# Kernel optimization log

Hardware: AMD Instinct MI355X
Metric: run time of the kernel (lower is better)

The kernel has to match this reference:

```python
import jax, jax.numpy as jnp
import numpy as np

GS = 128          # r_group_size
Q_MAX = 7.0       # 2**(q_bits-1)-1, q_bits=4
R_MAX = 7.0       # 2**(r_bits-1)-1, r_bits=4
R_MIN = -8.0      # -R_MAX-1
EPS = 1e-8


def _fake_quant_group(w, n_bits=4, group_size=128, eps=1e-8):
    # symmetric group-wise fake quant of the weight (done once at __init__)
    qmax = 2 ** (n_bits - 1) - 1
    qmin = -qmax - 1
    O, I = w.shape
    wg = w.reshape(O, I // group_size, group_size)
    scale = jnp.maximum(jnp.max(jnp.abs(wg), axis=-1, keepdims=True) / qmax, eps)
    wq = jnp.clip(jnp.round(wg / scale), qmin, qmax) * scale
    return wq.reshape(O, I)


def _select_pow2_base(t):
    # smallest value in {2,4,8,16,32,64} that is >= t (64 if none)
    base = jnp.full_like(t, 64.0)
    for v in (32.0, 16.0, 8.0, 4.0, 2.0):
        base = jnp.where(t <= v, jnp.full_like(t, v), base)
    return base


def setup_inputs() -> dict:
    key = jax.random.key(0)
    kx, kw, kb = jax.random.split(key, 3)
    B, S, IN, OUT = 4, 2048, 4096, 11008
    x = jax.random.normal(kx, (B, S, IN), dtype=jnp.float32)
    w_raw = jax.random.normal(kw, (OUT, IN), dtype=jnp.float32)
    weight = _fake_quant_group(w_raw, n_bits=4, group_size=128)
    bias = jax.random.normal(kb, (OUT,), dtype=jnp.float32)
    return {"x": x, "weight": weight, "bias": bias}


def reference(x, weight, bias):
    # dynamic quotient-remainder activation fake-quant (init path)
    H = x.shape[-1]
    xg = x.astype(jnp.float32).reshape(x.shape[:-1] + (H // GS, GS))  # [..., G, gs]
    max_abs = jnp.maximum(jnp.max(jnp.abs(xg), axis=-1, keepdims=True), EPS)
    base = _select_pow2_base(max_abs / Q_MAX)                 # [..., G, 1]
    q = jnp.clip(jnp.round(xg / base), -Q_MAX, Q_MAX)          # quotient
    r = xg - base * q                                          # remainder
    max_abs_r = jnp.maximum(jnp.max(jnp.abs(r), axis=-1, keepdims=True), EPS)
    scale_r = max_abs_r / R_MAX
    r_dq = jnp.clip(jnp.round(r / scale_r), R_MIN, R_MAX) * scale_r
    x_recon = (base * q + r_dq).reshape(x.shape)
    # F.linear: y = x @ W^T + b
    return jnp.einsum("bsi,oi->bso", x_recon, weight) + bias
```

## Files before the change

kernel.cpp:

```cpp
#include <hip/hip_runtime.h>
#include <stdint.h>
#include <stddef.h>

typedef __bf16 bf16x8 __attribute__((ext_vector_type(8)));
typedef float  f32x4  __attribute__((ext_vector_type(4)));
typedef float  f32x2  __attribute__((ext_vector_type(2)));

__device__ __forceinline__ unsigned short f2bf(float f) {
  unsigned int u = __builtin_bit_cast(unsigned int, f);
  u += 0x7fffu + ((u >> 16) & 1u);
  return (unsigned short)(u >> 16);
}

__device__ __forceinline__ void gld_lds16(const void* g, void* l) {
  __builtin_amdgcn_global_load_lds(
      (__attribute__((address_space(1))) void*)(g),
      (__attribute__((address_space(3))) void*)(l), 16, 0, 0);
}

#define BAR()     asm volatile("s_barrier" ::: "memory")
#define WAITVM(n) asm volatile("s_waitcnt vmcnt(" #n ")" ::: "memory")
#define SCHED0()  __builtin_amdgcn_sched_barrier(0)

__global__ __launch_bounds__(256) void quant_x_kernel(
    const float* __restrict__ x, unsigned short* __restrict__ xb, long long ngroups)
{
  const int lane = threadIdx.x & 63;
  const int wv   = threadIdx.x >> 6;
  long long g = (long long)blockIdx.x * 4 + wv;
  if (g >= ngroups) return;

  const float* xg = x + g * 128;
  f32x2 v = __builtin_nontemporal_load(
      reinterpret_cast<const f32x2*>(xg + lane * 2));

  float m = fmaxf(fabsf(v[0]), fabsf(v[1]));
  #pragma unroll
  for (int off = 32; off; off >>= 1) m = fmaxf(m, __shfl_xor(m, off));
  m = fmaxf(m, 1e-8f);

  float t = m / 7.0f;
  float base = t <= 2.f ? 2.f : t <= 4.f ? 4.f : t <= 8.f ? 8.f
             : t <= 16.f ? 16.f : t <= 32.f ? 32.f : 64.f;
  float inv_base = 1.0f / base;

  float q0 = fminf(fmaxf(rintf(v[0] * inv_base), -7.f), 7.f);
  float q1 = fminf(fmaxf(rintf(v[1] * inv_base), -7.f), 7.f);
  float r0 = v[0] - base * q0;
  float r1 = v[1] - base * q1;

  float mr = fmaxf(fabsf(r0), fabsf(r1));
  #pragma unroll
  for (int off = 32; off; off >>= 1) mr = fmaxf(mr, __shfl_xor(mr, off));
  mr = fmaxf(mr, 1e-8f);
  float scale_r = mr / 7.0f;

  float rd0 = fminf(fmaxf(rintf(r0 / scale_r), -8.f), 7.f) * scale_r;
  float rd1 = fminf(fmaxf(rintf(r1 / scale_r), -8.f), 7.f) * scale_r;

  float y0 = base * q0 + rd0;
  float y1 = base * q1 + rd1;

  unsigned int packed = (unsigned int)f2bf(y0) | ((unsigned int)f2bf(y1) << 16);
  *reinterpret_cast<unsigned int*>(xb + g * 128 + lane * 2) = packed;
}

__global__ __launch_bounds__(256) void cvt_w_kernel(
    const float* __restrict__ w, unsigned short* __restrict__ wb, long long n)
{
  long long i = ((long long)blockIdx.x * blockDim.x + threadIdx.x) * 8;
  if (i + 7 >= n) {
    if (i >= n) return;
    for (long long j = i; j < n; ++j) wb[j] = f2bf(w[j]);
    return;
  }
  f32x4 v0 = __builtin_nontemporal_load(reinterpret_cast<const f32x4*>(w + i));
  f32x4 v1 = __builtin_nontemporal_load(reinterpret_cast<const f32x4*>(w + i + 4));
  uint4 o;
  o.x = (unsigned)f2bf(v0[0]) | ((unsigned)f2bf(v0[1]) << 16);
  o.y = (unsigned)f2bf(v0[2]) | ((unsigned)f2bf(v0[3]) << 16);
  o.z = (unsigned)f2bf(v1[0]) | ((unsigned)f2bf(v1[1]) << 16);
  o.w = (unsigned)f2bf(v1[2]) | ((unsigned)f2bf(v1[3]) << 16);
  *reinterpret_cast<uint4*>(wb + i) = o;
}

#define BM 256
#define BN 256
#define BK 64

#define MFMA16(a, b, c) __builtin_amdgcn_mfma_f32_16x16x32_bf16(a, b, c, 0, 0, 0)

__global__ __launch_bounds__(512, 2) void gemm256_bias(
    const unsigned short* __restrict__ A,
    const unsigned short* __restrict__ B,
    const float* __restrict__ bias,
    float* __restrict__ C,
    int M, int N, int K)
{
  __shared__ unsigned short lds[2][2][2][128 * 64];

  const int tid  = threadIdx.x;
  const int lane = tid & 63;
  const int wid  = tid >> 6;
  const int wm   = wid >> 2;
  const int wn   = wid & 3;
  const int laneq = lane & 15;
  const int laneh = lane >> 4;
  const int lq7   = laneq & 7;

  const int ntm = M / BM;
  const int ntn = N / BN;
  int tm, tn;
  if ((ntm & 15) == 0) {
    int rem = blockIdx.x;
    int str = 0, stc = 0, w = 16;
    for (;;) {
      int w2 = (ntn - stc * 16 < 16) ? (ntn - stc * 16) : 16;
      int sz = 16 * w2;
      if (rem < sz) { w = w2; break; }
      rem -= sz;
      ++stc;
      if (stc * 16 >= ntn) { stc = 0; ++str; }
    }
    tm = str * 16 + rem / w;
    tn = stc * 16 + rem % w;
  } else {
    tm = (int)blockIdx.x / ntn;
    tn = (int)blockIdx.x % ntn;
  }
  const size_t m0 = (size_t)tm * BM;
  const size_t n0 = (size_t)tn * BN;

  const int NT = K / BK;

  const int ss0 = (laneh ^ lq7);
  const int ss1 = ((4 + laneh) ^ lq7);

  const char* ldsb = (const char*)&lds[0][0][0][0];
  const int aOff = wm * 16384 + laneq * 128;
  const int bOff = 32768 + (wn >> 1) * 16384 + ((wn & 1) * 64 + laneq) * 128;

  const int c0 = tid, c1 = 512 + tid;
  const int r0 = c0 >> 3, sl0 = (c0 & 7) ^ (r0 & 7);
  const int r1 = c1 >> 3, sl1 = (c1 & 7) ^ (r1 & 7);
  const unsigned short* gA0 = A + (m0 + r0) * (size_t)K + sl0 * 8;
  const unsigned short* gA1 = A + (m0 + r1) * (size_t)K + sl1 * 8;
  const unsigned short* gB0 = B + (n0 + r0) * (size_t)K + sl0 * 8;
  const unsigned short* gB1 = B + (n0 + r1) * (size_t)K + sl1 * 8;
  const size_t hstep = (size_t)128 * K;

  char* dst0 = (char*)ldsb + wid * 1024;
  char* dst1 = dst0 + 65536;

  f32x4 acc[8][4];
  #pragma unroll
  for (int i = 0; i < 8; i++)
    #pragma unroll
    for (int j = 0; j < 4; j++)
      acc[i][j] = (f32x4){0.f, 0.f, 0.f, 0.f};

  #define STAGETILE(kt, dstD)                                                \
    do {                                                                     \
      gld_lds16(gA0 + (size_t)(kt) * 64,          (dstD));                   \
      gld_lds16(gA1 + (size_t)(kt) * 64,          (dstD) + 8192);            \
      gld_lds16(gA0 + hstep + (size_t)(kt) * 64,  (dstD) + 16384);           \
      gld_lds16(gA1 + hstep + (size_t)(kt) * 64,  (dstD) + 16384 + 8192);    \
      gld_lds16(gB0 + (size_t)(kt) * 64,          (dstD) + 32768);           \
      gld_lds16(gB1 + (size_t)(kt) * 64,          (dstD) + 32768 + 8192);    \
      gld_lds16(gB0 + hstep + (size_t)(kt) * 64,  (dstD) + 49152);           \
      gld_lds16(gB1 + hstep + (size_t)(kt) * 64,  (dstD) + 49152 + 8192);    \
    } while (0)

  STAGETILE(0, dst0);
  WAITVM(0);
  BAR();

  bf16x8 al[4][2], ah[4][2], bl[2][2], bh[2][2];

  for (int t = 0; t < NT; ++t) {
    const int d = t & 1;
    const char* aS0 = ldsb + (d << 16) + aOff + ss0 * 16;
    const char* aS1 = ldsb + (d << 16) + aOff + ss1 * 16;
    const char* bS0 = ldsb + (d << 16) + bOff + ss0 * 16;
    const char* bS1 = ldsb + (d << 16) + bOff + ss1 * 16;

    if (t + 1 < NT) { char* dn = d ? dst0 : dst1; STAGETILE(t + 1, dn); }

    #pragma unroll
    for (int mi = 0; mi < 4; ++mi) {
      al[mi][0] = *(const bf16x8*)(aS0 + mi * 2048);
      al[mi][1] = *(const bf16x8*)(aS1 + mi * 2048);
    }
    #pragma unroll
    for (int nj = 0; nj < 2; ++nj) {
      bl[nj][0] = *(const bf16x8*)(bS0 + nj * 2048);
      bl[nj][1] = *(const bf16x8*)(bS1 + nj * 2048);
    }
    #pragma unroll
    for (int nj = 0; nj < 2; ++nj) {
      bh[nj][0] = *(const bf16x8*)(bS0 + 4096 + nj * 2048);
      bh[nj][1] = *(const bf16x8*)(bS1 + 4096 + nj * 2048);
    }
    #pragma unroll
    for (int mi = 0; mi < 4; ++mi) {
      ah[mi][0] = *(const bf16x8*)(aS0 + 8192 + mi * 2048);
      ah[mi][1] = *(const bf16x8*)(aS1 + 8192 + mi * 2048);
    }
    SCHED0();

    __builtin_amdgcn_s_setprio(1);
    #pragma unroll
    for (int mi = 0; mi < 4; ++mi)
      #pragma unroll
      for (int nj = 0; nj < 2; ++nj) {
        acc[mi][nj] = MFMA16(al[mi][0], bl[nj][0], acc[mi][nj]);
        acc[mi][nj] = MFMA16(al[mi][1], bl[nj][1], acc[mi][nj]);
      }
    SCHED0();
    #pragma unroll
    for (int mi = 0; mi < 4; ++mi)
      #pragma unroll
      for (int nj = 0; nj < 2; ++nj) {
        acc[mi][2 + nj] = MFMA16(al[mi][0], bh[nj][0], acc[mi][2 + nj]);
        acc[mi][2 + nj] = MFMA16(al[mi][1], bh[nj][1], acc[mi][2 + nj]);
      }
    SCHED0();
    #pragma unroll
    for (int mi = 0; mi < 4; ++mi)
      #pragma unroll
      for (int nj = 0; nj < 2; ++nj) {
        acc[4 + mi][2 + nj] = MFMA16(ah[mi][0], bh[nj][0], acc[4 + mi][2 + nj]);
        acc[4 + mi][2 + nj] = MFMA16(ah[mi][1], bh[nj][1], acc[4 + mi][2 + nj]);
      }
    #pragma unroll
    for (int mi = 0; mi < 4; ++mi)
      #pragma unroll
      for (int nj = 0; nj < 2; ++nj) {
        acc[4 + mi][nj] = MFMA16(ah[mi][0], bl[nj][0], acc[4 + mi][nj]);
        acc[4 + mi][nj] = MFMA16(ah[mi][1], bl[nj][1], acc[4 + mi][nj]);
      }
    __builtin_amdgcn_s_setprio(0);

    WAITVM(0);
    BAR();
  }
  #undef STAGETILE

  #pragma unroll
  for (int nj = 0; nj < 4; ++nj) {
    int col = (int)n0 + wn * 64 + nj * 16 + laneq;
    float bv = bias[col];
    #pragma unroll
    for (int mi = 0; mi < 8; ++mi) {
      size_t row = m0 + wm * 128 + mi * 16 + laneh * 4;
      float* cp = C + row * (size_t)N + col;
      #pragma unroll
      for (int r = 0; r < 4; ++r)
        __builtin_nontemporal_store(acc[mi][nj][r] + bv, cp + (size_t)r * N);
    }
  }
}

extern "C" void kernel_launch(void* const* d_in, const int* in_sizes, int n_in,
                              void* d_out, int out_size, void* d_ws, size_t ws_size,
                              hipStream_t stream) {
  const float* x    = (const float*)d_in[0];
  const float* w    = (const float*)d_in[1];
  const float* bias = (const float*)d_in[2];
  float* out = (float*)d_out;

  const long long xN = in_sizes[0];
  const long long wN = in_sizes[1];
  const int N = in_sizes[2];
  const int K = (int)(wN / N);
  const int M = (int)(xN / K);

  unsigned short* xb = (unsigned short*)d_ws;
  unsigned short* wb = xb + xN;

  long long ngroups = xN / 128;
  long long qblocks = (ngroups + 3) / 4;
  quant_x_kernel<<<(int)qblocks, 256, 0, stream>>>(x, xb, ngroups);

  long long cblocks = (wN + 2047) / 2048;
  cvt_w_kernel<<<(int)cblocks, 256, 0, stream>>>(w, wb, wN);

  int grid = (M / BM) * (N / BN);
  gemm256_bias<<<grid, 512, 0, stream>>>(xb, wb, bias, out, M, N, K);
}
```

Baseline: 763.3 us.

## Switch GEMM inner loop from 16x16x32 to 32x32x16 bf16 MFMA tiles

```diff
diff --git a/kernel.cpp b/kernel.cpp
--- a/kernel.cpp
+++ b/kernel.cpp
@@ -3,6 +3,7 @@
 #include <stddef.h>
 
 typedef __bf16 bf16x8 __attribute__((ext_vector_type(8)));
+typedef float  f32x16 __attribute__((ext_vector_type(16)));
 typedef float  f32x4  __attribute__((ext_vector_type(4)));
 typedef float  f32x2  __attribute__((ext_vector_type(2)));
 
@@ -88,7 +89,7 @@
 #define BN 256
 #define BK 64
 
-#define MFMA16(a, b, c) __builtin_amdgcn_mfma_f32_16x16x32_bf16(a, b, c, 0, 0, 0)
+#define MFMA32(a, b, c) __builtin_amdgcn_mfma_f32_32x32x16_bf16(a, b, c, 0, 0, 0)
 
 __global__ __launch_bounds__(512, 2) void gemm256_bias(
     const unsigned short* __restrict__ A,
@@ -104,9 +105,8 @@
   const int wid  = tid >> 6;
   const int wm   = wid >> 2;
   const int wn   = wid & 3;
-  const int laneq = lane & 15;
-  const int laneh = lane >> 4;
-  const int lq7   = laneq & 7;
+  const int l31  = lane & 31;
+  const int lk   = lane >> 5;
 
   const int ntm = M / BM;
   const int ntn = N / BN;
@@ -133,12 +133,13 @@
 
   const int NT = K / BK;
 
-  const int ss0 = (laneh ^ lq7);
-  const int ss1 = ((4 + laneh) ^ lq7);
+  const int r7 = l31 & 7;
+  const int sl_ks[4] = { ((0 * 2 + lk) ^ r7) * 16, ((1 * 2 + lk) ^ r7) * 16,
+                         ((2 * 2 + lk) ^ r7) * 16, ((3 * 2 + lk) ^ r7) * 16 };
 
   const char* ldsb = (const char*)&lds[0][0][0][0];
-  const int aOff = wm * 16384 + laneq * 128;
-  const int bOff = 32768 + (wn >> 1) * 16384 + ((wn & 1) * 64 + laneq) * 128;
+  const int aOff = wm * 16384 + l31 * 128;
+  const int bOff = 32768 + (wn >> 1) * 16384 + ((wn & 1) * 64 + l31) * 128;
 
   const int c0 = tid, c1 = 512 + tid;
   const int r0 = c0 >> 3, sl0 = (c0 & 7) ^ (r0 & 7);
@@ -152,12 +153,12 @@
   char* dst0 = (char*)ldsb + wid * 1024;
   char* dst1 = dst0 + 65536;
 
-  f32x4 acc[8][4];
-  #pragma unroll
-  for (int i = 0; i < 8; i++)
-    #pragma unroll
-    for (int j = 0; j < 4; j++)
-      acc[i][j] = (f32x4){0.f, 0.f, 0.f, 0.f};
+  f32x16 acc[4][2];
+  #pragma unroll
+  for (int i = 0; i < 4; i++)
+    #pragma unroll
+    for (int j = 0; j < 2; j++)
+      acc[i][j] = (f32x16)(0.f);
 
   #define STAGETILE(kt, dstD)                                                \
     do {                                                                     \
@@ -175,70 +176,37 @@
   WAITVM(0);
   BAR();
 
-  bf16x8 al[4][2], ah[4][2], bl[2][2], bh[2][2];
+  bf16x8 af[4][4], bf[2][4];
 
   for (int t = 0; t < NT; ++t) {
     const int d = t & 1;
-    const char* aS0 = ldsb + (d << 16) + aOff + ss0 * 16;
-    const char* aS1 = ldsb + (d << 16) + aOff + ss1 * 16;
-    const char* bS0 = ldsb + (d << 16) + bOff + ss0 * 16;
-    const char* bS1 = ldsb + (d << 16) + bOff + ss1 * 16;
+    const char* aB = ldsb + (d << 16) + aOff;
+    const char* bB = ldsb + (d << 16) + bOff;
 
     if (t + 1 < NT) { char* dn = d ? dst0 : dst1; STAGETILE(t + 1, dn); }
 
     #pragma unroll
-    for (int mi = 0; mi < 4; ++mi) {
-      al[mi][0] = *(const bf16x8*)(aS0 + mi * 2048);
-      al[mi][1] = *(const bf16x8*)(aS1 + mi * 2048);
-    }
-    #pragma unroll
-    for (int nj = 0; nj < 2; ++nj) {
-      bl[nj][0] = *(const bf16x8*)(bS0 + nj * 2048);
-      bl[nj][1] = *(const bf16x8*)(bS1 + nj * 2048);
-    }
-    #pragma unroll
-    for (int nj = 0; nj < 2; ++nj) {
-      bh[nj][0] = *(const bf16x8*)(bS0 + 4096 + nj * 2048);
-      bh[nj][1] = *(const bf16x8*)(bS1 + 4096 + nj * 2048);
-    }
-    #pragma unroll
-    for (int mi = 0; mi < 4; ++mi) {
-      ah[mi][0] = *(const bf16x8*)(aS0 + 8192 + mi * 2048);
-      ah[mi][1] = *(const bf16x8*)(aS1 + 8192 + mi * 2048);
+    for (int ks = 0; ks < 4; ++ks) {
+      const int so = sl_ks[ks];
+      #pragma unroll
+      for (int mi = 0; mi < 4; ++mi)
+        af[mi][ks] = *(const bf16x8*)(aB + mi * 4096 + so);
+      #pragma unroll
+      for (int nj = 0; nj < 2; ++nj)
+        bf[nj][ks] = *(const bf16x8*)(bB + nj * 4096 + so);
     }
     SCHED0();
 
     __builtin_amdgcn_s_setprio(1);
     #pragma unroll
-    for (int mi = 0; mi < 4; ++mi)
-      #pragma unroll
-      for (int nj = 0; nj < 2; ++nj) {
-        acc[mi][nj] = MFMA16(al[mi][0], bl[nj][0], acc[mi][nj]);
-        acc[mi][nj] = MFMA16(al[mi][1], bl[nj][1], acc[mi][nj]);
-      }
-    SCHED0();
-    #pragma unroll
-    for (int mi = 0; mi < 4; ++mi)
-      #pragma unroll
-      for (int nj = 0; nj < 2; ++nj) {
-        acc[mi][2 + nj] = MFMA16(al[mi][0], bh[nj][0], acc[mi][2 + nj]);
-        acc[mi][2 + nj] = MFMA16(al[mi][1], bh[nj][1], acc[mi][2 + nj]);
-      }
-    SCHED0();
-    #pragma unroll
-    for (int mi = 0; mi < 4; ++mi)
-      #pragma unroll
-      for (int nj = 0; nj < 2; ++nj) {
-        acc[4 + mi][2 + nj] = MFMA16(ah[mi][0], bh[nj][0], acc[4 + mi][2 + nj]);
-        acc[4 + mi][2 + nj] = MFMA16(ah[mi][1], bh[nj][1], acc[4 + mi][2 + nj]);
-      }
-    #pragma unroll
-    for (int mi = 0; mi < 4; ++mi)
-      #pragma unroll
-      for (int nj = 0; nj < 2; ++nj) {
-        acc[4 + mi][nj] = MFMA16(ah[mi][0], bl[nj][0], acc[4 + mi][nj]);
-        acc[4 + mi][nj] = MFMA16(ah[mi][1], bl[nj][1], acc[4 + mi][nj]);
-      }
+    for (int ks = 0; ks < 4; ++ks) {
+      #pragma unroll
+      for (int mi = 0; mi < 4; ++mi)
+        #pragma unroll
+        for (int nj = 0; nj < 2; ++nj)
+          acc[mi][nj] = MFMA32(af[mi][ks], bf[nj][ks], acc[mi][nj]);
+      SCHED0();
+    }
     __builtin_amdgcn_s_setprio(0);
 
     WAITVM(0);
@@ -247,16 +215,20 @@
   #undef STAGETILE
 
   #pragma unroll
-  for (int nj = 0; nj < 4; ++nj) {
-    int col = (int)n0 + wn * 64 + nj * 16 + laneq;
+  for (int nj = 0; nj < 2; ++nj) {
+    int col = (int)n0 + wn * 64 + nj * 32 + l31;
     float bv = bias[col];
     #pragma unroll
-    for (int mi = 0; mi < 8; ++mi) {
-      size_t row = m0 + wm * 128 + mi * 16 + laneh * 4;
-      float* cp = C + row * (size_t)N + col;
-      #pragma unroll
-      for (int r = 0; r < 4; ++r)
-        __builtin_nontemporal_store(acc[mi][nj][r] + bv, cp + (size_t)r * N);
+    for (int mi = 0; mi < 4; ++mi) {
+      size_t rbase = m0 + wm * 128 + mi * 32 + 4 * lk;
+      #pragma unroll
+      for (int rg = 0; rg < 4; ++rg) {
+        float* cp = C + (rbase + 8 * rg) * (size_t)N + col;
+        #pragma unroll
+        for (int rr = 0; rr < 4; ++rr)
+          __builtin_nontemporal_store(acc[mi][nj][rg * 4 + rr] + bv,
+                                      cp + (size_t)rr * N);
+      }
     }
   }
 }
```

Result: slower. 846.1 us (+10.8%).
